# Kernel optimization log

Hardware: AMD Instinct MI355X
Metric: run time of the kernel (lower is better)

Reference implementation:

```python
import math
import jax, jax.numpy as jnp
import numpy as np

NSAMPLE = 16
HEADS = 4
ATTN = 256
EPS = 1e-5


def setup_inputs() -> dict:
    key = jax.random.key(0)
    ks = jax.random.split(key, 16)
    B, N, M, C = 2, 4096, 4096, 128

    def w(k, shape):
        return jax.random.normal(k, shape, jnp.float32) / np.sqrt(shape[-1]).astype(np.float32)

    return dict(
        pos1=jax.random.normal(ks[0], (B, 3, N), jnp.float32),
        pos2=jax.random.normal(ks[1], (B, 3, M), jnp.float32),
        feature1=jax.random.normal(ks[2], (B, C, N), jnp.float32),
        feature2=jax.random.normal(ks[3], (B, C, M), jnp.float32),
        w0=w(ks[4], (128, 2 * C + 3)), g0=jnp.ones(128), b0=jnp.zeros(128),
        w1=w(ks[5], (128, 128)), g1=jnp.ones(128), b1=jnp.zeros(128),
        w2=w(ks[6], (256, 128)), g2=jnp.ones(256), b2=jnp.zeros(256),
        qw=w(ks[7], (ATTN, 512)), qb=jnp.zeros(ATTN),
        kw=w(ks[8], (ATTN, C)), kb=jnp.zeros(ATTN),
        vw=w(ks[9], (ATTN, C)), vb=jnp.zeros(ATTN),
        ow=w(ks[10], (512, ATTN)), ob=jnp.zeros(512),
        lng=jnp.ones(512), lnb=jnp.zeros(512),
        fw=w(ks[11], (256, 512)), fb=jnp.zeros(256),
    )


def _knn_idx(p1t, p2t, k):
    # p1t: (B,N,3) queries; p2t: (B,M,3) keys. k nearest in pos2 for each pos1 point.
    d = (jnp.sum(p1t * p1t, -1, keepdims=True)
         - 2.0 * jnp.einsum('bnd,bmd->bnm', p1t, p2t)
         + jnp.sum(p2t * p2t, -1)[:, None, :])
    _, idx = jax.lax.top_k(-d, k)  # (B,N,k)
    return idx


def reference(pos1, pos2, feature1, feature2,
              w0, g0, b0, w1, g1, b1, w2, g2, b2,
              qw, qb, kw, kb, vw, vb, ow, ob, lng, lnb, fw, fb):
    B, _, N = pos1.shape
    M = pos2.shape[2]
    p1t = pos1.transpose(0, 2, 1)  # (B,N,3)
    p2t = pos2.transpose(0, 2, 1)  # (B,M,3)
    idx = _knn_idx(p1t, p2t, NSAMPLE)  # (B,N,k)

    gather = jax.vmap(lambda f, i: f[i])  # (M,C),(N,k)->(N,k,C)
    pos_diff = gather(p2t, idx) - p1t[:, :, None, :]              # (B,N,k,3)
    f2g = gather(feature2.transpose(0, 2, 1), idx)                # (B,N,k,C)
    f1r = jnp.broadcast_to(feature1.transpose(0, 2, 1)[:, :, None, :], f2g.shape)
    x = jnp.concatenate([pos_diff, f2g, f1r], -1)                 # (B,N,k,2C+3)

    # 1x1 conv + BatchNorm (training-mode batch stats, biased var) + ReLU
    for w, g, b in ((w0, g0, b0), (w1, g1, b1), (w2, g2, b2)):
        x = jnp.einsum('bnkc,oc->bnko', x, w)
        mu = x.mean((0, 1, 2))
        var = x.var((0, 1, 2))
        x = jax.nn.relu((x - mu) * jax.lax.rsqrt(var + EPS) * g + b)

    feat = jnp.concatenate([x.max(2), x.mean(2)], -1)  # (B,N,2*mlp[-1])

    hd = ATTN // HEADS
    f2t = feature2.transpose(0, 2, 1)  # (B,M,C)
    Q = (feat @ qw.T + qb).reshape(B, N, HEADS, hd).transpose(0, 2, 1, 3)
    K = (f2t @ kw.T + kb).reshape(B, M, HEADS, hd).transpose(0, 2, 1, 3)
    V = (f2t @ vw.T + vb).reshape(B, M, HEADS, hd).transpose(0, 2, 1, 3)
    attn = jax.nn.softmax(jnp.einsum('bhnd,bhmd->bhnm', Q, K) / math.sqrt(hd), axis=-1)
    o = jnp.einsum('bhnm,bhmd->bhnd', attn, V).transpose(0, 2, 1, 3).reshape(B, N, ATTN)
    o = o @ ow.T + ob

    y = feat + o
    mu = y.mean(-1, keepdims=True)
    var = y.var(-1, keepdims=True)
    y = (y - mu) * jax.lax.rsqrt(var + EPS) * lng + lnb
    y = y @ fw.T + fb                      # (B,N,mlp[-1])
    return (pos1, y.transpose(0, 2, 1))    # (B,3,N), (B,mlp[-1],N)
```

## Files before the change

### kernel.cpp

```cpp
#include <hip/hip_runtime.h>
#include <hip/hip_bf16.h>

constexpr int B_ = 2, N_ = 4096, M_ = 4096, C_ = 128;

typedef __attribute__((ext_vector_type(8))) __bf16 bf16x8;
typedef __attribute__((ext_vector_type(4))) float f32x4;

__global__ __launch_bounds__(256) void knn_part_kernel(const float* __restrict__ pos1,
                                                       const float* __restrict__ pos2,
                                                       float* __restrict__ pd,
                                                       int* __restrict__ pi) {
  __shared__ float tX[256], tY[256], tZ[256], tS[256];
  int tid = threadIdx.x;
  int bn = blockIdx.x * 256 + tid;
  int b = bn >> 12, n = bn & 4095;
  int seg = blockIdx.y;
  const float* p1 = pos1 + (long)b * 3 * N_;
  float qx = p1[n], qy = p1[N_ + n], qz = p1[2 * N_ + n];
  float s1 = __fadd_rn(__fadd_rn(__fmul_rn(qx, qx), __fmul_rn(qy, qy)), __fmul_rn(qz, qz));
  const float* p2 = pos2 + (long)b * 3 * M_ + seg * 256;
  {
    float x = p2[tid], y = p2[M_ + tid], z = p2[2 * M_ + tid];
    tX[tid] = x; tY[tid] = y; tZ[tid] = z;
    tS[tid] = __fadd_rn(__fadd_rn(__fmul_rn(x, x), __fmul_rn(y, y)), __fmul_rn(z, z));
  }
  __syncthreads();
  float rd[16]; int ri[16];
#pragma unroll
  for (int k = 0; k < 16; k++) { rd[k] = 3.0e38f; ri[k] = 0; }
  for (int mm = 0; mm < 256; mm += 8) {
    float dv[8];
#pragma unroll
    for (int u = 0; u < 8; u++) {
      float e = __fmaf_rn(qz, tZ[mm + u],
                          __fmaf_rn(qy, tY[mm + u], __fmul_rn(qx, tX[mm + u])));
      dv[u] = __fadd_rn(__fsub_rn(s1, __fadd_rn(e, e)), tS[mm + u]);
    }
    float thr = rd[15];
    bool any = false;
#pragma unroll
    for (int u = 0; u < 8; u++) any = any || (dv[u] < thr);
    if (any) {
#pragma unroll
      for (int u = 0; u < 8; u++) {
        float d = dv[u];
        if (d < rd[15]) {
          float cd = d; int ci = seg * 256 + mm + u;
#pragma unroll
          for (int k = 0; k < 16; k++) {
            bool lt = cd < rd[k];
            float td = lt ? rd[k] : cd;
            int ti = lt ? ri[k] : ci;
            rd[k] = lt ? cd : rd[k];
            ri[k] = lt ? ci : ri[k];
            cd = td; ci = ti;
          }
        }
      }
    }
  }
  long base = (long)seg * 16 * 8192 + bn;
#pragma unroll
  for (int k = 0; k < 16; k++) {
    pd[base + (long)k * 8192] = rd[k];
    pi[base + (long)k * 8192] = ri[k];
  }
}

__global__ __launch_bounds__(256) void knn_merge_kernel(const float* __restrict__ pd,
                                                        const int* __restrict__ pi,
                                                        int* __restrict__ idx) {
  int bn = blockIdx.x * 256 + threadIdx.x;
  float rd[16]; int ri[16];
#pragma unroll
  for (int k = 0; k < 16; k++) { rd[k] = 3.0e38f; ri[k] = 0; }
  for (int seg = 0; seg < 16; seg++) {
    for (int k = 0; k < 16; k++) {
      float d = pd[((long)seg * 16 + k) * 8192 + bn];
      if (d >= rd[15]) break;
      int ci = pi[((long)seg * 16 + k) * 8192 + bn];
      float cd = d;
#pragma unroll
      for (int j = 0; j < 16; j++) {
        bool lt = cd < rd[j];
        float td = lt ? rd[j] : cd;
        int ti = lt ? ri[j] : ci;
        rd[j] = lt ? cd : rd[j];
        ri[j] = lt ? ci : ri[j];
        cd = td; ci = ti;
      }
    }
  }
#pragma unroll
  for (int k = 0; k < 16; k++) idx[(long)bn * 16 + k] = ri[k];
}

__global__ __launch_bounds__(128) void g131_kernel(const float* __restrict__ pos,
                                                   const float* __restrict__ feat,
                                                   const float* __restrict__ w0,
                                                   float* __restrict__ out,
                                                   float sign, int woff) {
  __shared__ float Xs[131 * 16];
  int tid = threadIdx.x;
  long b = blockIdx.x >> 8;
  int i0 = (blockIdx.x & 255) * 16;
  for (int e = tid; e < 131 * 16; e += 128) {
    int r = e & 15, c = e >> 4;
    float v = (c < 3) ? sign * pos[b * 3 * N_ + (long)c * N_ + i0 + r]
                      : feat[b * C_ * N_ + (long)(c - 3) * N_ + i0 + r];
    Xs[c * 16 + r] = v;
  }
  __syncthreads();
  int o = tid;
  float acc[16];
#pragma unroll
  for (int r = 0; r < 16; r++) acc[r] = 0.f;
  for (int c = 0; c < 131; c++) {
    float wv = w0[(long)o * 259 + (c < 3 ? c : (woff + c - 3))];
    const float* xr = &Xs[c * 16];
#pragma unroll
    for (int r = 0; r < 16; r++) acc[r] = fmaf(xr[r], wv, acc[r]);
  }
#pragma unroll
  for (int r = 0; r < 16; r++) out[((b << 12) + i0 + r) * 128 + o] = acc[r];
}

__global__ __launch_bounds__(256) void z0stats_kernel(const int* __restrict__ idx,
                                                      const float* __restrict__ A1,
                                                      const float* __restrict__ A2,
                                                      double* __restrict__ st) {
  int tid = threadIdx.x;
  int o = tid & 127, half = tid >> 7;
  float sum = 0.f, sq = 0.f;
  int g0 = blockIdx.x * 32;
  for (int gi = 0; gi < 32; gi++) {
    int bn = g0 + gi;
    long b = bn >> 12;
    float a1 = A1[(long)bn * 128 + o];
    for (int k = half; k < 16; k += 2) {
      int m = idx[bn * 16 + k];
      float v = A2[(b * 4096 + m) * 128 + o] + a1;
      sum += v;
      sq += v * v;
    }
  }
  __shared__ float ls[256], lq[256];
  ls[tid] = sum; lq[tid] = sq;
  __syncthreads();
  if (tid < 128) {
    atomicAdd(&st[o], (double)(ls[tid] + ls[tid + 128]));
    atomicAdd(&st[128 + o], (double)(lq[tid] + lq[tid + 128]));
  }
}

__global__ __launch_bounds__(256) void statsb_kernel(const __hip_bfloat16* __restrict__ Z,
                                                     long nrows, double* __restrict__ st) {
  int tid = threadIdx.x;
  int c = tid & 127, sub = tid >> 7;
  long slot = (long)blockIdx.x * 2 + sub;
  long stride = (long)gridDim.x * 2;
  float sum = 0.f, sq = 0.f;
  for (long r = slot; r < nrows; r += stride) {
    float v = __bfloat162float(Z[r * 128 + c]);
    sum += v;
    sq += v * v;
  }
  __shared__ float ls[256], lq[256];
  ls[tid] = sum; lq[tid] = sq;
  __syncthreads();
  if (tid < 128) {
    atomicAdd(&st[c], (double)(ls[tid] + ls[tid + 128]));
    atomicAdd(&st[128 + c], (double)(lq[tid] + lq[tid + 128]));
  }
}

__global__ void bnfin_kernel(const double* __restrict__ st, const float* __restrict__ g,
                             const float* __restrict__ bb, float* __restrict__ sc,
                             float* __restrict__ sh, int CO, double inv) {
  int c = threadIdx.x;
  if (c < CO) {
    double mu = st[c] * inv;
    double var = st[CO + c] * inv - mu * mu;
    double rstd = 1.0 / sqrt(var + 1e-5);
    double scv = (double)g[c] * rstd;
    sc[c] = (float)scv;
    sh[c] = (float)((double)bb[c] - mu * scv);
  }
}

__global__ __launch_bounds__(256) void gemm1_mfma_kernel(
    const float* __restrict__ A2, const float* __restrict__ A1,
    const int* __restrict__ idxp, const float* __restrict__ w1,
    const float* __restrict__ sc0, const float* __restrict__ sh0,
    __hip_bfloat16* __restrict__ z1b) {
  __shared__ unsigned short As[64 * 136];
  __shared__ unsigned short Bs[64 * 136];
  __shared__ float scs[128], shs[128];
  int tid = threadIdx.x;
  int lane = tid & 63, w = tid >> 6;
  int cb = blockIdx.x;
  long r0 = (long)blockIdx.y * 64;
  int c0 = cb * 64;
  if (tid < 128) { scs[tid] = sc0[tid]; shs[tid] = sh0[tid]; }
  __syncthreads();
  {
    int row = tid >> 2, kb = (tid & 3) * 32;
    long g = r0 + row;
    int m = idxp[g];
    const float* a2p = &A2[(((g >> 16) << 12) + m) * 128 + kb];
    const float* a1p = &A1[(g >> 4) * 128 + kb];
    unsigned short* ap = &As[row * 136 + kb];
    const float* wp = &w1[(long)(c0 + row) * 128 + kb];
    unsigned short* bp = &Bs[row * 136 + kb];
#pragma unroll
    for (int h = 0; h < 4; h++) {
      union { unsigned short u[8]; uint4 v; } oa, ob;
#pragma unroll
      for (int j = 0; j < 8; j++) {
        int k = kb + h * 8 + j;
        float raw = a2p[h * 8 + j] + a1p[h * 8 + j];
        float v = fmaxf(0.f, fmaf(raw, scs[k], shs[k]));
        oa.u[j] = __bfloat16_as_ushort(__float2bfloat16(v));
        ob.u[j] = __bfloat16_as_ushort(__float2bfloat16(wp[h * 8 + j]));
      }
      *reinterpret_cast<uint4*>(ap + h * 8) = oa.v;
      *reinterpret_cast<uint4*>(bp + h * 8) = ob.v;
    }
  }
  __syncthreads();

  int fr = lane & 15, fk = (lane >> 4) * 8;
  bf16x8 a[4];
#pragma unroll
  for (int kk = 0; kk < 4; kk++)
    a[kk] = *reinterpret_cast<const bf16x8*>(&As[(w * 16 + fr) * 136 + kk * 32 + fk]);
  f32x4 acc[4];
#pragma unroll
  for (int n2 = 0; n2 < 4; n2++) {
    acc[n2] = (f32x4){0.f, 0.f, 0.f, 0.f};
#pragma unroll
    for (int kk = 0; kk < 4; kk++) {
      bf16x8 bfrag = *reinterpret_cast<const bf16x8*>(&Bs[(n2 * 16 + fr) * 136 + kk * 32 + fk]);
      acc[n2] = __builtin_amdgcn_mfma_f32_16x16x32_bf16(a[kk], bfrag, acc[n2], 0, 0, 0);
    }
  }
#pragma unroll
  for (int n2 = 0; n2 < 4; n2++) {
#pragma unroll
    for (int r = 0; r < 4; r++) {
      long row = r0 + w * 16 + (lane >> 4) * 4 + r;
      z1b[row * 128 + c0 + n2 * 16 + fr] = __float2bfloat16(acc[n2][r]);
    }
  }
}

template <int EPI>
__global__ __launch_bounds__(256) void gemm2_mfma_kernel(
    const __hip_bfloat16* __restrict__ z1b, const float* __restrict__ w2,
    const float* __restrict__ sc1, const float* __restrict__ sh1,
    const float* __restrict__ sc2, const float* __restrict__ sh2,
    float* __restrict__ feat, double* __restrict__ st) {
  __shared__ unsigned short As[64 * 136];
  __shared__ unsigned short Bs[64 * 136];
  __shared__ float scs[128], shs[128];
  __shared__ float Sred[4 * 64], Qred[4 * 64];
  int tid = threadIdx.x;
  int lane = tid & 63, w = tid >> 6;
  int cb = blockIdx.x;
  long r0 = (long)blockIdx.y * 64;
  int c0 = cb * 64;
  if (tid < 128) { scs[tid] = sc1[tid]; shs[tid] = sh1[tid]; }
  __syncthreads();
  {
    int row = tid >> 2, kb = (tid & 3) * 32;
    const __hip_bfloat16* zp = &z1b[(r0 + row) * 128 + kb];
    unsigned short* ap = &As[row * 136 + kb];
    const float* wp = &w2[(long)(c0 + row) * 128 + kb];
    unsigned short* bp = &Bs[row * 136 + kb];
#pragma unroll
    for (int h = 0; h < 4; h++) {
      union { unsigned short u[8]; uint4 v; } in, oa, ob;
      in.v = *reinterpret_cast<const uint4*>(zp + h * 8);
#pragma unroll
      for (int j = 0; j < 8; j++) {
        int k = kb + h * 8 + j;
        float f = __bfloat162float(__ushort_as_bfloat16(in.u[j]));
        float v = fmaxf(0.f, fmaf(f, scs[k], shs[k]));
        oa.u[j] = __bfloat16_as_ushort(__float2bfloat16(v));
        ob.u[j] = __bfloat16_as_ushort(__float2bfloat16(wp[h * 8 + j]));
      }
      *reinterpret_cast<uint4*>(ap + h * 8) = oa.v;
      *reinterpret_cast<uint4*>(bp + h * 8) = ob.v;
    }
  }
  __syncthreads();

  int fr = lane & 15, fk = (lane >> 4) * 8;
  bf16x8 a[4];
#pragma unroll
  for (int kk = 0; kk < 4; kk++)
    a[kk] = *reinterpret_cast<const bf16x8*>(&As[(w * 16 + fr) * 136 + kk * 32 + fk]);
  f32x4 acc[4];
#pragma unroll
  for (int n2 = 0; n2 < 4; n2++) {
    acc[n2] = (f32x4){0.f, 0.f, 0.f, 0.f};
#pragma unroll
    for (int kk = 0; kk < 4; kk++) {
      bf16x8 bfrag = *reinterpret_cast<const bf16x8*>(&Bs[(n2 * 16 + fr) * 136 + kk * 32 + fk]);
      acc[n2] = __builtin_amdgcn_mfma_f32_16x16x32_bf16(a[kk], bfrag, acc[n2], 0, 0, 0);
    }
  }

  if (EPI == 4) {
#pragma unroll
    for (int n2 = 0; n2 < 4; n2++) {
      float s = 0.f, q = 0.f;
#pragma unroll
      for (int r = 0; r < 4; r++) { s += acc[n2][r]; q += acc[n2][r] * acc[n2][r]; }
      s += __shfl_xor(s, 16); s += __shfl_xor(s, 32);
      q += __shfl_xor(q, 16); q += __shfl_xor(q, 32);
      if (lane < 16) { Sred[w * 64 + n2 * 16 + fr] = s; Qred[w * 64 + n2 * 16 + fr] = q; }
    }
    __syncthreads();
    if (tid < 64) {
      float S = Sred[tid] + Sred[64 + tid] + Sred[128 + tid] + Sred[192 + tid];
      float Q = Qred[tid] + Qred[64 + tid] + Qred[128 + tid] + Qred[192 + tid];
      atomicAdd(&st[c0 + tid], (double)S);
      atomicAdd(&st[256 + c0 + tid], (double)Q);
    }
  } else {
    int bn = (int)(r0 >> 4) + w;
#pragma unroll
    for (int n2 = 0; n2 < 4; n2++) {
      int c = c0 + n2 * 16 + fr;
      float scv = sc2[c], shv = sh2[c];
      float mx = -1e30f, sm = 0.f;
#pragma unroll
      for (int r = 0; r < 4; r++) {
        float v = fmaxf(0.f, fmaf(acc[n2][r], scv, shv));
        mx = fmaxf(mx, v);
        sm += v;
      }
      mx = fmaxf(mx, __shfl_xor(mx, 16)); mx = fmaxf(mx, __shfl_xor(mx, 32));
      sm += __shfl_xor(sm, 16); sm += __shfl_xor(sm, 32);
      if (lane < 16) {
        feat[(long)bn * 512 + c] = mx;
        feat[(long)bn * 512 + 256 + c] = sm * (1.f / 16.f);
      }
    }
  }
}

template <int EPI, int XM, bool BN>
__global__ __launch_bounds__(256) void gemm_kernel(
    const void* __restrict__ Xv, const float* __restrict__ W, float* __restrict__ out,
    int K, int CO, const float* __restrict__ bias, const float* __restrict__ sc,
    const float* __restrict__ sh, const float* __restrict__ res,
    __hip_bfloat16* __restrict__ obf, const float* __restrict__ A1,
    const int* __restrict__ idxp, double* __restrict__ st) {
  __shared__ float S[2][32 * 68];
  int tid = threadIdx.x;
  int tx = tid & 15, ty = tid >> 4;
  int cb = blockIdx.x;
  long r0 = (long)blockIdx.y * 64;
  int c0 = cb * 64;
  float acc[4][4];
#pragma unroll
  for (int i = 0; i < 4; i++)
#pragma unroll
    for (int j = 0; j < 4; j++) acc[i][j] = 0.f;

  for (int k0 = 0; k0 < K; k0 += 32) {
    if (XM != 1) {
      int c = tid & 31, rr = tid >> 5;
      float scv = 0.f, shv = 0.f;
      if (BN) { scv = sc[k0 + c]; shv = sh[k0 + c]; }
#pragma unroll
      for (int i = 0; i < 8; i++) {
        int r = rr + i * 8;
        long g = r0 + r;
        float v = ((const float*)Xv)[g * K + k0 + c];
        if (BN) v = fmaxf(0.f, fmaf(v, scv, shv));
        S[0][c * 68 + r] = v;
      }
    } else {
      int m = tid & 63, cc = tid >> 6;
      long b = r0 >> 12;
      long mg = (r0 & 4095) + m;
#pragma unroll
      for (int i = 0; i < 8; i++) {
        int c = cc + i * 4;
        S[0][c * 68 + m] = ((const float*)Xv)[(b * K + k0 + c) * 4096 + mg];
      }
    }
    {
      int c = tid & 31, oo = tid >> 5;
#pragma unroll
      for (int i = 0; i < 8; i++) {
        int o = oo + i * 8;
        S[1][c * 68 + o] = W[(long)(c0 + o) * K + k0 + c];
      }
    }
    __syncthreads();
#pragma unroll
    for (int kk = 0; kk < 32; kk++) {
      float4 a = *reinterpret_cast<const float4*>(&S[0][kk * 68 + ty * 4]);
      float4 bv = *reinterpret_cast<const float4*>(&S[1][kk * 68 + tx * 4]);
      float av[4] = {a.x, a.y, a.z, a.w};
      float bw[4] = {bv.x, bv.y, bv.z, bv.w};
#pragma unroll
      for (int i = 0; i < 4; i++)
#pragma unroll
        for (int j = 0; j < 4; j++) acc[i][j] = fmaf(av[i], bw[j], acc[i][j]);
    }
    __syncthreads();
  }

  if (EPI == 2) {
    const float4 b4 = *reinterpret_cast<const float4*>(&bias[c0 + tx * 4]);
#pragma unroll
    for (int i = 0; i < 4; i++) {
      long r = r0 + ty * 4 + i;
      float4 f4 = *reinterpret_cast<const float4*>(&res[r * CO + c0 + tx * 4]);
      float4 o4 = make_float4(acc[i][0] + b4.x + f4.x, acc[i][1] + b4.y + f4.y,
                              acc[i][2] + b4.z + f4.z, acc[i][3] + b4.w + f4.w);
      *reinterpret_cast<float4*>(&out[r * CO + c0 + tx * 4]) = o4;
    }
  } else if (EPI == 3) {
    float* Sf = &S[0][0];
#pragma unroll
    for (int j = 0; j < 4; j++) {
      float bj = bias[c0 + tx * 4 + j];
      float4 colv = make_float4(acc[0][j] + bj, acc[1][j] + bj, acc[2][j] + bj,
                                acc[3][j] + bj);
      *reinterpret_cast<float4*>(&Sf[(tx * 4 + j) * 68 + ty * 4]) = colv;
    }
    __syncthreads();
    long b = r0 >> 12;
    long n0 = (r0 & 4095);
    int n = tid & 63, oo = tid >> 6;
#pragma unroll
    for (int i = 0; i < 16; i++) {
      int o = oo + i * 4;
      out[(b * CO + c0 + o) * 4096L + n0 + n] = Sf[o * 68 + n];
    }
  } else if (EPI == 7) {
    long b = r0 >> 12;
    long nn = (r0 & 4095) + ty * 4;
    const float4 b4 = *reinterpret_cast<const float4*>(&bias[c0 + tx * 4]);
    __hip_bfloat16* Ob = obf + ((b * (CO >> 6) + cb) * 4096L) * 64;
#pragma unroll
    for (int i = 0; i < 4; i++) {
      union { unsigned short u[4]; uint2 v; } pk;
      pk.u[0] = __bfloat16_as_ushort(__float2bfloat16(acc[i][0] + b4.x));
      pk.u[1] = __bfloat16_as_ushort(__float2bfloat16(acc[i][1] + b4.y));
      pk.u[2] = __bfloat16_as_ushort(__float2bfloat16(acc[i][2] + b4.z));
      pk.u[3] = __bfloat16_as_ushort(__float2bfloat16(acc[i][3] + b4.w));
      *reinterpret_cast<uint2*>(&Ob[(nn + i) * 64 + tx * 4]) = pk.v;
    }
  } else if (EPI == 8) {
    float* Sf = &S[0][0];
#pragma unroll
    for (int j = 0; j < 4; j++) {
      float bj = bias[c0 + tx * 4 + j];
      float4 colv = make_float4(acc[0][j] + bj, acc[1][j] + bj, acc[2][j] + bj,
                                acc[3][j] + bj);
      *reinterpret_cast<float4*>(&Sf[(tx * 4 + j) * 68 + ty * 4]) = colv;
    }
    __syncthreads();
    long b = r0 >> 12;
    long n0 = (r0 & 4095);
    int n = tid & 63, oo = tid >> 6;
#pragma unroll
    for (int i = 0; i < 16; i++) {
      int o = oo + i * 4;
      obf[((b * 4 + cb) * 64 + o) * 4096L + n0 + n] = __float2bfloat16(Sf[o * 68 + n]);
    }
  }
}

__global__ __launch_bounds__(256) void flash_mfma_kernel(
    const __hip_bfloat16* __restrict__ Q, const __hip_bfloat16* __restrict__ Kb,
    const __hip_bfloat16* __restrict__ Vtg, float* __restrict__ Opart,
    float* __restrict__ mbuf, float* __restrict__ lbuf) {
  __shared__ unsigned short Ks[64 * 72];
  __shared__ unsigned short Vt[64 * 72];
  __shared__ unsigned short Ps[4][16 * 72];
  int tid = threadIdx.x;
  int lane = tid & 63, w = tid >> 6;
  int bh = blockIdx.x >> 6;
  int qt = blockIdx.x & 63;
  int half = blockIdx.y;
  long base = (long)bh * 4096 * 64;
  int row0 = qt * 64 + w * 16;
  int fr = lane & 15;
  int fk = (lane >> 4) * 8;

  bf16x8 aq[2];
#pragma unroll
  for (int kk = 0; kk < 2; kk++)
    aq[kk] = *reinterpret_cast<const bf16x8*>(&Q[base + (long)(row0 + fr) * 64 + kk * 32 + fk]);

  f32x4 o[4];
#pragma unroll
  for (int i = 0; i < 4; i++) o[i] = (f32x4){0.f, 0.f, 0.f, 0.f};
  float m_run[4], l_run[4];
#pragma unroll
  for (int r = 0; r < 4; r++) { m_run[r] = -3.0e38f; l_run[r] = 0.f; }

  int skey = tid >> 2, sdc = (tid & 3) * 16;
  int vd = tid & 63, vkg = tid >> 6;
  int vsw = (vd ^ (vd >> 3)) & 7;

  int mstart = half * 2048;
  for (int m0 = mstart; m0 < mstart + 2048; m0 += 64) {
    __syncthreads();
    {
      const __hip_bfloat16* kp = &Kb[base + (long)(m0 + skey) * 64 + sdc];
      *reinterpret_cast<uint4*>(&Ks[skey * 72 + sdc]) =
          *reinterpret_cast<const uint4*>(kp);
      *reinterpret_cast<uint4*>(&Ks[skey * 72 + sdc + 8]) =
          *reinterpret_cast<const uint4*>(kp + 8);
#pragma unroll
      for (int j8 = 0; j8 < 2; j8++) {
        int k0 = vkg * 16 + j8 * 8;
        int kb = k0 >> 3;
        *reinterpret_cast<uint4*>(&Vt[vd * 72 + ((kb ^ vsw) << 3)]) =
            *reinterpret_cast<const uint4*>(&Vtg[base + (long)vd * 4096 + m0 + k0]);
      }
    }
    __syncthreads();

    f32x4 s[4];
#pragma unroll
    for (int n = 0; n < 4; n++) {
      s[n] = (f32x4){0.f, 0.f, 0.f, 0.f};
#pragma unroll
      for (int kk = 0; kk < 2; kk++) {
        bf16x8 bk = *reinterpret_cast<const bf16x8*>(&Ks[(n * 16 + fr) * 72 + kk * 32 + fk]);
        s[n] = __builtin_amdgcn_mfma_f32_16x16x32_bf16(aq[kk], bk, s[n], 0, 0, 0);
      }
    }

    float p[4][4];
#pragma unroll
    for (int r = 0; r < 4; r++) {
      float sv0 = s[0][r] * 0.125f, sv1 = s[1][r] * 0.125f;
      float sv2 = s[2][r] * 0.125f, sv3 = s[3][r] * 0.125f;
      float mx = fmaxf(fmaxf(sv0, sv1), fmaxf(sv2, sv3));
      mx = fmaxf(mx, __shfl_xor(mx, 1));
      mx = fmaxf(mx, __shfl_xor(mx, 2));
      mx = fmaxf(mx, __shfl_xor(mx, 4));
      mx = fmaxf(mx, __shfl_xor(mx, 8));
      float mn = fmaxf(m_run[r], mx);
      float fac = __expf(m_run[r] - mn);
      p[0][r] = __expf(sv0 - mn);
      p[1][r] = __expf(sv1 - mn);
      p[2][r] = __expf(sv2 - mn);
      p[3][r] = __expf(sv3 - mn);
      float rs = (p[0][r] + p[1][r]) + (p[2][r] + p[3][r]);
      rs += __shfl_xor(rs, 1);
      rs += __shfl_xor(rs, 2);
      rs += __shfl_xor(rs, 4);
      rs += __shfl_xor(rs, 8);
      l_run[r] = l_run[r] * fac + rs;
      m_run[r] = mn;
#pragma unroll
      for (int n2 = 0; n2 < 4; n2++) o[n2][r] *= fac;
    }

    unsigned short* pw = &Ps[w][0];
#pragma unroll
    for (int r = 0; r < 4; r++) {
      int prow = (lane >> 4) * 4 + r;
#pragma unroll
      for (int n = 0; n < 4; n++)
        pw[prow * 72 + n * 16 + fr] = __bfloat16_as_ushort(__float2bfloat16(p[n][r]));
    }
    bf16x8 ap[2];
#pragma unroll
    for (int kk = 0; kk < 2; kk++)
      ap[kk] = *reinterpret_cast<const bf16x8*>(&pw[fr * 72 + kk * 32 + fk]);

#pragma unroll
    for (int n2 = 0; n2 < 4; n2++) {
      int d = n2 * 16 + fr;
      int dsw = (d ^ (d >> 3)) & 7;
#pragma unroll
      for (int kk = 0; kk < 2; kk++) {
        int kb = kk * 4 + (lane >> 4);
        bf16x8 bv = *reinterpret_cast<const bf16x8*>(&Vt[d * 72 + ((kb ^ dsw) << 3)]);
        o[n2] = __builtin_amdgcn_mfma_f32_16x16x32_bf16(ap[kk], bv, o[n2], 0, 0, 0);
      }
    }
  }

  int b = bh >> 2, h = bh & 3;
  float* Op = Opart + (long)half * 2097152;
#pragma unroll
  for (int r = 0; r < 4; r++) {
    float inv = 1.f / l_run[r];
    int qrow = qt * 64 + w * 16 + (lane >> 4) * 4 + r;
    long nrow = (long)(b * 4096 + qrow);
#pragma unroll
    for (int n2 = 0; n2 < 4; n2++) {
      Op[nrow * 256 + h * 64 + n2 * 16 + fr] = o[n2][r] * inv;
    }
    if (fr == 0) {
      long mlrow = ((long)(half * 8 + bh)) * 4096 + qrow;
      mbuf[mlrow] = m_run[r];
      lbuf[mlrow] = l_run[r];
    }
  }
}

__global__ __launch_bounds__(256) void flash_merge_kernel(
    const float* __restrict__ Opart, const float* __restrict__ mbuf,
    const float* __restrict__ lbuf, float* __restrict__ O) {
  long r = blockIdx.x;
  int c = threadIdx.x;
  int b = (int)(r >> 12);
  int n = (int)(r & 4095);
  int h = c >> 6;
  int bh = b * 4 + h;
  long ml0 = ((long)(0 * 8 + bh)) * 4096 + n;
  long ml1 = ((long)(1 * 8 + bh)) * 4096 + n;
  float m0 = mbuf[ml0], l0 = lbuf[ml0];
  float m1 = mbuf[ml1], l1 = lbuf[ml1];
  float M = fmaxf(m0, m1);
  float w0 = l0 * __expf(m0 - M);
  float w1 = l1 * __expf(m1 - M);
  float invden = 1.f / (w0 + w1);
  float o0 = Opart[r * 256 + c];
  float o1 = Opart[2097152 + r * 256 + c];
  O[r * 256 + c] = (o0 * w0 + o1 * w1) * invden;
}

__global__ __launch_bounds__(256) void ln_kernel(float* __restrict__ y,
                                                 const float* __restrict__ lng,
                                                 const float* __restrict__ lnb) {
  long r = blockIdx.x;
  int tid = threadIdx.x;
  float v0 = y[r * 512 + tid];
  float v1 = y[r * 512 + 256 + tid];
  float s = v0 + v1;
  float q = v0 * v0 + v1 * v1;
#pragma unroll
  for (int off = 1; off < 64; off <<= 1) {
    s += __shfl_xor(s, off);
    q += __shfl_xor(q, off);
  }
  __shared__ float red[8];
  __shared__ float mv[2];
  int w = tid >> 6;
  if ((tid & 63) == 0) { red[w] = s; red[4 + w] = q; }
  __syncthreads();
  if (tid == 0) {
    float S = red[0] + red[1] + red[2] + red[3];
    float Q2 = red[4] + red[5] + red[6] + red[7];
    float mu = S * (1.f / 512.f);
    float var = Q2 * (1.f / 512.f) - mu * mu;
    mv[0] = mu;
    mv[1] = rsqrtf(var + 1e-5f);
  }
  __syncthreads();
  float mu = mv[0], rstd = mv[1];
  y[r * 512 + tid] = (v0 - mu) * rstd * lng[tid] + lnb[tid];
  y[r * 512 + 256 + tid] = (v1 - mu) * rstd * lng[256 + tid] + lnb[256 + tid];
}

__global__ void poscopy_kernel(const float* __restrict__ p, float* __restrict__ o) {
  int i = blockIdx.x * 256 + threadIdx.x;
  o[i] = p[i];
}

extern "C" void kernel_launch(void* const* d_in, const int* in_sizes, int n_in,
                              void* d_out, int out_size, void* d_ws, size_t ws_size,
                              hipStream_t stream) {
  (void)in_sizes; (void)n_in; (void)out_size; (void)ws_size;
  const float* pos1 = (const float*)d_in[0];
  const float* pos2 = (const float*)d_in[1];
  const float* f1 = (const float*)d_in[2];
  const float* f2 = (const float*)d_in[3];
  const float* w0 = (const float*)d_in[4];
  const float* g0 = (const float*)d_in[5];
  const float* b0 = (const float*)d_in[6];
  const float* w1 = (const float*)d_in[7];
  const float* g1 = (const float*)d_in[8];
  const float* b1 = (const float*)d_in[9];
  const float* w2 = (const float*)d_in[10];
  const float* g2 = (const float*)d_in[11];
  const float* b2 = (const float*)d_in[12];
  const float* qw = (const float*)d_in[13];
  const float* qb = (const float*)d_in[14];
  const float* kw = (const float*)d_in[15];
  const float* kb = (const float*)d_in[16];
  const float* vw = (const float*)d_in[17];
  const float* vb = (const float*)d_in[18];
  const float* ow = (const float*)d_in[19];
  const float* obv = (const float*)d_in[20];
  const float* lng = (const float*)d_in[21];
  const float* lnb = (const float*)d_in[22];
  const float* fw = (const float*)d_in[23];
  const float* fb = (const float*)d_in[24];

  char* ws = (char*)d_ws;
  __hip_bfloat16* z1b = (__hip_bfloat16*)(ws);
  __hip_bfloat16* Qbf = (__hip_bfloat16*)(ws);
  __hip_bfloat16* Kbf = (__hip_bfloat16*)(ws + (8ull << 20));
  __hip_bfloat16* Vtg = (__hip_bfloat16*)(ws + (16ull << 20));
  float* attno = (float*)(ws + (24ull << 20));
  float* y0 = (float*)(ws);
  int* idx = (int*)(ws + (32ull << 20));
  float* A1 = (float*)(ws + (33ull << 20));
  float* A2 = (float*)(ws + (37ull << 20));
  float* feat = (float*)(ws + (32ull << 20));
  char* statp = ws + (48ull << 20);
  float* mbuf = (float*)(ws + (49ull << 20));
  float* lbuf = (float*)(ws + (50ull << 20));
  float* pd = (float*)(ws + (56ull << 20));
  int* pi = (int*)(ws + (64ull << 20));
  float* Opart = (float*)(ws + (56ull << 20));
  double* st0 = (double*)(statp);
  double* st1 = (double*)(statp + 2048);
  double* st2 = (double*)(statp + 4096);
  float* sc0 = (float*)(statp + 8192);
  float* sh0 = (float*)(statp + 8704);
  float* sc1 = (float*)(statp + 9216);
  float* sh1 = (float*)(statp + 9728);
  float* sc2 = (float*)(statp + 10240);
  float* sh2 = (float*)(statp + 11264);

  float* out0 = (float*)d_out;
  float* out1 = out0 + 24576;

  hipMemsetAsync(statp, 0, 8192, stream);

  knn_part_kernel<<<dim3(32, 16), 256, 0, stream>>>(pos1, pos2, pd, pi);
  knn_merge_kernel<<<32, 256, 0, stream>>>(pd, pi, idx);
  g131_kernel<<<512, 128, 0, stream>>>(pos2, f2, w0, A2, 1.f, 3);
  g131_kernel<<<512, 128, 0, stream>>>(pos1, f1, w0, A1, -1.f, 131);
  z0stats_kernel<<<256, 256, 0, stream>>>(idx, A1, A2, st0);
  bnfin_kernel<<<1, 256, 0, stream>>>(st0, g0, b0, sc0, sh0, 128, 1.0 / 131072.0);
  gemm1_mfma_kernel<<<dim3(2, 2048), 256, 0, stream>>>(
      A2, A1, idx, w1, sc0, sh0, z1b);
  statsb_kernel<<<512, 256, 0, stream>>>(z1b, 131072L, st1);
  bnfin_kernel<<<1, 256, 0, stream>>>(st1, g1, b1, sc1, sh1, 128, 1.0 / 131072.0);
  gemm2_mfma_kernel<4><<<dim3(4, 2048), 256, 0, stream>>>(
      z1b, w2, sc1, sh1, nullptr, nullptr, nullptr, st2);
  bnfin_kernel<<<1, 256, 0, stream>>>(st2, g2, b2, sc2, sh2, 256, 1.0 / 131072.0);
  gemm2_mfma_kernel<5><<<dim3(4, 2048), 256, 0, stream>>>(
      z1b, w2, sc1, sh1, sc2, sh2, feat, nullptr);
  gemm_kernel<7, 0, false><<<dim3(4, 128), 256, 0, stream>>>(
      feat, qw, nullptr, 512, 256, qb, nullptr, nullptr, nullptr, Qbf, nullptr, nullptr, nullptr);
  gemm_kernel<7, 1, false><<<dim3(4, 128), 256, 0, stream>>>(
      f2, kw, nullptr, 128, 256, kb, nullptr, nullptr, nullptr, Kbf, nullptr, nullptr, nullptr);
  gemm_kernel<8, 1, false><<<dim3(4, 128), 256, 0, stream>>>(
      f2, vw, nullptr, 128, 256, vb, nullptr, nullptr, nullptr, Vtg, nullptr, nullptr, nullptr);
  flash_mfma_kernel<<<dim3(512, 2), 256, 0, stream>>>(Qbf, Kbf, Vtg, Opart, mbuf, lbuf);
  flash_merge_kernel<<<8192, 256, 0, stream>>>(Opart, mbuf, lbuf, attno);
  gemm_kernel<2, 0, false><<<dim3(8, 128), 256, 0, stream>>>(
      attno, ow, y0, 256, 512, obv, nullptr, nullptr, feat, nullptr, nullptr, nullptr, nullptr);
  ln_kernel<<<8192, 256, 0, stream>>>(y0, lng, lnb);
  gemm_kernel<3, 0, false><<<dim3(4, 128), 256, 0, stream>>>(
      y0, fw, out1, 512, 256, fb, nullptr, nullptr, nullptr, nullptr, nullptr, nullptr, nullptr);
  poscopy_kernel<<<96, 256, 0, stream>>>(pos1, out0);
}
```

Measured before the change: 792.5 us.

## Replace FP32 SIMT dense GEMMs with bf16 MFMA GEMM kernel

Replaces the scalar FP32 tiled GEMM used for the Q/K/V projections, output projection and final FFN with a kernel that converts operands to bf16 in shared memory and uses 16x16x32 bf16 MFMA instructions. The K-tile grows to 64 and the epilogues are rewritten for the MFMA accumulator layout. This cuts the FMA cost of these projection GEMMs, at the cost of bf16 rounding on inputs and weights for the output projection and final layer, which were previously computed in FP32.

```diff
diff --git a/kernel.cpp b/kernel.cpp
--- a/kernel.cpp
+++ b/kernel.cpp
@@ -351,89 +351,107 @@
   }
 }
 
-template <int EPI, int XM, bool BN>
-__global__ __launch_bounds__(256) void gemm_kernel(
-    const void* __restrict__ Xv, const float* __restrict__ W, float* __restrict__ out,
-    int K, int CO, const float* __restrict__ bias, const float* __restrict__ sc,
-    const float* __restrict__ sh, const float* __restrict__ res,
-    __hip_bfloat16* __restrict__ obf, const float* __restrict__ A1,
-    const int* __restrict__ idxp, double* __restrict__ st) {
-  __shared__ float S[2][32 * 68];
-  int tid = threadIdx.x;
-  int tx = tid & 15, ty = tid >> 4;
+template <int EPI, int XM>
+__global__ __launch_bounds__(256) void gemmA_mfma_kernel(
+    const float* __restrict__ X, const float* __restrict__ W, int K, int CO,
+    const float* __restrict__ bias, const float* __restrict__ res,
+    float* __restrict__ outf, __hip_bfloat16* __restrict__ outb) {
+  __shared__ unsigned short As[64 * 136];
+  __shared__ unsigned short Bs[64 * 136];
+  int tid = threadIdx.x;
+  int lane = tid & 63, w = tid >> 6;
   int cb = blockIdx.x;
   long r0 = (long)blockIdx.y * 64;
   int c0 = cb * 64;
-  float acc[4][4];
-#pragma unroll
-  for (int i = 0; i < 4; i++)
-#pragma unroll
-    for (int j = 0; j < 4; j++) acc[i][j] = 0.f;
-
-  for (int k0 = 0; k0 < K; k0 += 32) {
-    if (XM != 1) {
-      int c = tid & 31, rr = tid >> 5;
-      float scv = 0.f, shv = 0.f;
-      if (BN) { scv = sc[k0 + c]; shv = sh[k0 + c]; }
-#pragma unroll
-      for (int i = 0; i < 8; i++) {
-        int r = rr + i * 8;
-        long g = r0 + r;
-        float v = ((const float*)Xv)[g * K + k0 + c];
-        if (BN) v = fmaxf(0.f, fmaf(v, scv, shv));
-        S[0][c * 68 + r] = v;
+  int fr = lane & 15, fk = (lane >> 4) * 8;
+  f32x4 acc[4];
+#pragma unroll
+  for (int n2 = 0; n2 < 4; n2++) acc[n2] = (f32x4){0.f, 0.f, 0.f, 0.f};
+
+  for (int k0 = 0; k0 < K; k0 += 64) {
+    if (XM == 0) {
+      int row = tid >> 2, kb = (tid & 3) * 16;
+      const float* xp = &X[(r0 + row) * K + k0 + kb];
+      unsigned short* ap = &As[row * 136 + kb];
+#pragma unroll
+      for (int h = 0; h < 2; h++) {
+        union { unsigned short u[8]; uint4 v; } oa;
+#pragma unroll
+        for (int j = 0; j < 8; j++)
+          oa.u[j] = __bfloat16_as_ushort(__float2bfloat16(xp[h * 8 + j]));
+        *reinterpret_cast<uint4*>(ap + h * 8) = oa.v;
       }
     } else {
       int m = tid & 63, cc = tid >> 6;
       long b = r0 >> 12;
       long mg = (r0 & 4095) + m;
 #pragma unroll
-      for (int i = 0; i < 8; i++) {
+      for (int i = 0; i < 16; i++) {
         int c = cc + i * 4;
-        S[0][c * 68 + m] = ((const float*)Xv)[(b * K + k0 + c) * 4096 + mg];
+        As[m * 136 + c] =
+            __bfloat16_as_ushort(__float2bfloat16(X[(b * K + k0 + c) * 4096 + mg]));
       }
     }
     {
-      int c = tid & 31, oo = tid >> 5;
-#pragma unroll
-      for (int i = 0; i < 8; i++) {
-        int o = oo + i * 8;
-        S[1][c * 68 + o] = W[(long)(c0 + o) * K + k0 + c];
+      int row = tid >> 2, kb = (tid & 3) * 16;
+      const float* wp = &W[(long)(c0 + row) * K + k0 + kb];
+      unsigned short* bp = &Bs[row * 136 + kb];
+#pragma unroll
+      for (int h = 0; h < 2; h++) {
+        union { unsigned short u[8]; uint4 v; } ob;
+#pragma unroll
+        for (int j = 0; j < 8; j++)
+          ob.u[j] = __bfloat16_as_ushort(__float2bfloat16(wp[h * 8 + j]));
+        *reinterpret_cast<uint4*>(bp + h * 8) = ob.v;
       }
     }
     __syncthreads();
-#pragma unroll
-    for (int kk = 0; kk < 32; kk++) {
-      float4 a = *reinterpret_cast<const float4*>(&S[0][kk * 68 + ty * 4]);
-      float4 bv = *reinterpret_cast<const float4*>(&S[1][kk * 68 + tx * 4]);
-      float av[4] = {a.x, a.y, a.z, a.w};
-      float bw[4] = {bv.x, bv.y, bv.z, bv.w};
-#pragma unroll
-      for (int i = 0; i < 4; i++)
-#pragma unroll
-        for (int j = 0; j < 4; j++) acc[i][j] = fmaf(av[i], bw[j], acc[i][j]);
+    bf16x8 a[2];
+#pragma unroll
+    for (int kk = 0; kk < 2; kk++)
+      a[kk] = *reinterpret_cast<const bf16x8*>(&As[(w * 16 + fr) * 136 + kk * 32 + fk]);
+#pragma unroll
+    for (int n2 = 0; n2 < 4; n2++) {
+#pragma unroll
+      for (int kk = 0; kk < 2; kk++) {
+        bf16x8 bfrag =
+            *reinterpret_cast<const bf16x8*>(&Bs[(n2 * 16 + fr) * 136 + kk * 32 + fk]);
+        acc[n2] = __builtin_amdgcn_mfma_f32_16x16x32_bf16(a[kk], bfrag, acc[n2], 0, 0, 0);
+      }
     }
     __syncthreads();
   }
 
   if (EPI == 2) {
-    const float4 b4 = *reinterpret_cast<const float4*>(&bias[c0 + tx * 4]);
-#pragma unroll
-    for (int i = 0; i < 4; i++) {
-      long r = r0 + ty * 4 + i;
-      float4 f4 = *reinterpret_cast<const float4*>(&res[r * CO + c0 + tx * 4]);
-      float4 o4 = make_float4(acc[i][0] + b4.x + f4.x, acc[i][1] + b4.y + f4.y,
-                              acc[i][2] + b4.z + f4.z, acc[i][3] + b4.w + f4.w);
-      *reinterpret_cast<float4*>(&out[r * CO + c0 + tx * 4]) = o4;
-    }
-  } else if (EPI == 3) {
-    float* Sf = &S[0][0];
-#pragma unroll
-    for (int j = 0; j < 4; j++) {
-      float bj = bias[c0 + tx * 4 + j];
-      float4 colv = make_float4(acc[0][j] + bj, acc[1][j] + bj, acc[2][j] + bj,
-                                acc[3][j] + bj);
-      *reinterpret_cast<float4*>(&Sf[(tx * 4 + j) * 68 + ty * 4]) = colv;
+#pragma unroll
+    for (int n2 = 0; n2 < 4; n2++) {
+      int col = c0 + n2 * 16 + fr;
+      float bv = bias[col];
+#pragma unroll
+      for (int r = 0; r < 4; r++) {
+        long row = r0 + w * 16 + (lane >> 4) * 4 + r;
+        outf[row * CO + col] = acc[n2][r] + bv + res[row * CO + col];
+      }
+    }
+  } else if (EPI == 7) {
+    long b = r0 >> 12;
+    int qbase = (int)(r0 & 4095) + w * 16 + (lane >> 4) * 4;
+    __hip_bfloat16* Ob = outb + ((b * 4 + cb) * 4096L) * 64;
+#pragma unroll
+    for (int n2 = 0; n2 < 4; n2++) {
+      float bv = bias[c0 + n2 * 16 + fr];
+#pragma unroll
+      for (int r = 0; r < 4; r++)
+        Ob[(long)(qbase + r) * 64 + n2 * 16 + fr] = __float2bfloat16(acc[n2][r] + bv);
+    }
+  } else {
+    float* Sf = (float*)As;
+#pragma unroll
+    for (int n2 = 0; n2 < 4; n2++) {
+      float bv = bias[c0 + n2 * 16 + fr];
+#pragma unroll
+      for (int r = 0; r < 4; r++)
+        Sf[(n2 * 16 + fr) * 68 + w * 16 + (lane >> 4) * 4 + r] = acc[n2][r] + bv;
     }
     __syncthreads();
     long b = r0 >> 12;
@@ -442,39 +460,10 @@
 #pragma unroll
     for (int i = 0; i < 16; i++) {
       int o = oo + i * 4;
-      out[(b * CO + c0 + o) * 4096L + n0 + n] = Sf[o * 68 + n];
-    }
-  } else if (EPI == 7) {
-    long b = r0 >> 12;
-    long nn = (r0 & 4095) + ty * 4;
-    const float4 b4 = *reinterpret_cast<const float4*>(&bias[c0 + tx * 4]);
-    __hip_bfloat16* Ob = obf + ((b * (CO >> 6) + cb) * 4096L) * 64;
-#pragma unroll
-    for (int i = 0; i < 4; i++) {
-      union { unsigned short u[4]; uint2 v; } pk;
-      pk.u[0] = __bfloat16_as_ushort(__float2bfloat16(acc[i][0] + b4.x));
-      pk.u[1] = __bfloat16_as_ushort(__float2bfloat16(acc[i][1] + b4.y));
-      pk.u[2] = __bfloat16_as_ushort(__float2bfloat16(acc[i][2] + b4.z));
-      pk.u[3] = __bfloat16_as_ushort(__float2bfloat16(acc[i][3] + b4.w));
-      *reinterpret_cast<uint2*>(&Ob[(nn + i) * 64 + tx * 4]) = pk.v;
-    }
-  } else if (EPI == 8) {
-    float* Sf = &S[0][0];
-#pragma unroll
-    for (int j = 0; j < 4; j++) {
-      float bj = bias[c0 + tx * 4 + j];
-      float4 colv = make_float4(acc[0][j] + bj, acc[1][j] + bj, acc[2][j] + bj,
-                                acc[3][j] + bj);
-      *reinterpret_cast<float4*>(&Sf[(tx * 4 + j) * 68 + ty * 4]) = colv;
-    }
-    __syncthreads();
-    long b = r0 >> 12;
-    long n0 = (r0 & 4095);
-    int n = tid & 63, oo = tid >> 6;
-#pragma unroll
-    for (int i = 0; i < 16; i++) {
-      int o = oo + i * 4;
-      obf[((b * 4 + cb) * 64 + o) * 4096L + n0 + n] = __float2bfloat16(Sf[o * 68 + n]);
+      if (EPI == 3)
+        outf[(b * CO + c0 + o) * 4096L + n0 + n] = Sf[o * 68 + n];
+      else
+        outb[((b * 4 + cb) * 64 + o) * 4096L + n0 + n] = __float2bfloat16(Sf[o * 68 + n]);
     }
   }
 }
@@ -751,18 +740,18 @@
   bnfin_kernel<<<1, 256, 0, stream>>>(st2, g2, b2, sc2, sh2, 256, 1.0 / 131072.0);
   gemm2_mfma_kernel<5><<<dim3(4, 2048), 256, 0, stream>>>(
       z1b, w2, sc1, sh1, sc2, sh2, feat, nullptr);
-  gemm_kernel<7, 0, false><<<dim3(4, 128), 256, 0, stream>>>(
-      feat, qw, nullptr, 512, 256, qb, nullptr, nullptr, nullptr, Qbf, nullptr, nullptr, nullptr);
-  gemm_kernel<7, 1, false><<<dim3(4, 128), 256, 0, stream>>>(
-      f2, kw, nullptr, 128, 256, kb, nullptr, nullptr, nullptr, Kbf, nullptr, nullptr, nullptr);
-  gemm_kernel<8, 1, false><<<dim3(4, 128), 256, 0, stream>>>(
-      f2, vw, nullptr, 128, 256, vb, nullptr, nullptr, nullptr, Vtg, nullptr, nullptr, nullptr);
+  gemmA_mfma_kernel<7, 0><<<dim3(4, 128), 256, 0, stream>>>(
+      feat, qw, 512, 256, qb, nullptr, nullptr, Qbf);
+  gemmA_mfma_kernel<7, 1><<<dim3(4, 128), 256, 0, stream>>>(
+      f2, kw, 128, 256, kb, nullptr, nullptr, Kbf);
+  gemmA_mfma_kernel<8, 1><<<dim3(4, 128), 256, 0, stream>>>(
+      f2, vw, 128, 256, vb, nullptr, nullptr, Vtg);
   flash_mfma_kernel<<<dim3(512, 2), 256, 0, stream>>>(Qbf, Kbf, Vtg, Opart, mbuf, lbuf);
   flash_merge_kernel<<<8192, 256, 0, stream>>>(Opart, mbuf, lbuf, attno);
-  gemm_kernel<2, 0, false><<<dim3(8, 128), 256, 0, stream>>>(
-      attno, ow, y0, 256, 512, obv, nullptr, nullptr, feat, nullptr, nullptr, nullptr, nullptr);
+  gemmA_mfma_kernel<2, 0><<<dim3(8, 128), 256, 0, stream>>>(
+      attno, ow, 256, 512, obv, feat, y0, nullptr);
   ln_kernel<<<8192, 256, 0, stream>>>(y0, lng, lnb);
-  gemm_kernel<3, 0, false><<<dim3(4, 128), 256, 0, stream>>>(
-      y0, fw, out1, 512, 256, fb, nullptr, nullptr, nullptr, nullptr, nullptr, nullptr, nullptr);
+  gemmA_mfma_kernel<3, 0><<<dim3(4, 128), 256, 0, stream>>>(
+      y0, fw, 512, 256, fb, nullptr, out1, nullptr);
   poscopy_kernel<<<96, 256, 0, stream>>>(pos1, out0);
 }
```

New measurement: 724.1 us. -8.6%, faster.
